# Kernel optimization log

Measured on AMD Instinct MI355X. Metric: run time of the kernel, lower is better.

The kernel has to match this reference:

```python
import jax, jax.numpy as jnp
import numpy as np

QMAX = 127.0

def quantize_int8(x):
    # symmetric per-row (per-token) int8 quantization
    scale = jnp.max(jnp.abs(x), axis=-1, keepdims=True) / QMAX  # [N,1]
    scale = jnp.maximum(scale, 1e-8)
    q = jnp.clip(jnp.round(x / scale), -QMAX, QMAX).astype(jnp.int8)
    return q, scale


def setup_inputs() -> dict:
    key = jax.random.key(0)
    k1, k2 = jax.random.split(key)
    in_features, out_features = 4096, 4096
    x = jax.random.normal(k1, (4, 2048, in_features), dtype=jnp.float32)
    # weight buffer: randint(1, 128) int8, shape (out, in)
    weight = jax.random.randint(k2, (out_features, in_features), 1, 128, dtype=jnp.int32).astype(jnp.int8)
    weight_scale = jnp.ones((1,), dtype=jnp.float32)
    return {"x": x, "weight": weight, "weight_scale": weight_scale}


def reference(x, weight, weight_scale):
    x_shape = x.shape
    xf = x.reshape(-1, x_shape[-1])  # [N, in]
    q, scale_x = quantize_int8(xf)
    acc = jnp.matmul(q, weight.T, preferred_element_type=jnp.int32)  # [N, out]
    y = acc.astype(jnp.float32) * scale_x * weight_scale[0]
    return y.reshape(*x_shape[:-1], -1)
```

## Files before the change

kernel.cpp:

```cpp
#include <hip/hip_runtime.h>
#include <cstdint>

typedef int v4i __attribute__((ext_vector_type(4)));

#define K_DIM 4096
#define BM 128
#define BN 128
#define BK 64

__global__ __launch_bounds__(256) void pack_weight(
    const int* __restrict__ w32, int8_t* __restrict__ w8, int total16)
{
    const int i = blockIdx.x * 256 + threadIdx.x;
    if (i >= total16) return;
    const v4i* src = reinterpret_cast<const v4i*>(w32) + i * 4;
    v4i out;
#pragma unroll
    for (int j = 0; j < 4; ++j) {
        const v4i v = src[j];
        out[j] = (v.x & 0xff) | ((v.y & 0xff) << 8) |
                 ((v.z & 0xff) << 16) | ((unsigned)(v.w & 0xff) << 24);
    }
    reinterpret_cast<v4i*>(w8)[i] = out;
}

__global__ __launch_bounds__(256) void quant_rows(
    const float* __restrict__ x, int8_t* __restrict__ q,
    float* __restrict__ scales)
{
    const int row = blockIdx.x;
    const int t   = threadIdx.x;
    const float4* xr4 = reinterpret_cast<const float4*>(x + (size_t)row * K_DIM);

    float4 v[4];
    float m = 0.0f;
#pragma unroll
    for (int i = 0; i < 4; ++i) {
        v[i] = xr4[i * 256 + t];
        m = fmaxf(m, fmaxf(fmaxf(fabsf(v[i].x), fabsf(v[i].y)),
                           fmaxf(fabsf(v[i].z), fabsf(v[i].w))));
    }
#pragma unroll
    for (int off = 32; off >= 1; off >>= 1)
        m = fmaxf(m, __shfl_xor(m, off, 64));

    __shared__ float wmax[4];
    if ((t & 63) == 0) wmax[t >> 6] = m;
    __syncthreads();
    const float am = fmaxf(fmaxf(wmax[0], wmax[1]), fmaxf(wmax[2], wmax[3]));
    const float s  = fmaxf(am / 127.0f, 1e-8f);
    if (t == 0) scales[row] = s;

    int* qi = reinterpret_cast<int*>(q + (size_t)row * K_DIM);
#pragma unroll
    for (int i = 0; i < 4; ++i) {
        const float e[4] = {v[i].x, v[i].y, v[i].z, v[i].w};
        unsigned packed = 0;
#pragma unroll
        for (int j = 0; j < 4; ++j) {
            float r = rintf(e[j] / s);
            r = fminf(fmaxf(r, -127.0f), 127.0f);
            packed |= ((unsigned)((int)r & 0xff)) << (8 * j);
        }
        qi[i * 256 + t] = (int)packed;
    }
}

__global__ __launch_bounds__(256, 2) void gemm_i8(
    const int8_t* __restrict__ A,
    const int8_t* __restrict__ B,
    const float* __restrict__ sA,
    const float* __restrict__ wsc,
    float* __restrict__ C,
    int M, int N)
{
    __shared__ int8_t ldsA[BM * BK];
    __shared__ int8_t ldsB[BN * BK];

    const int t    = threadIdx.x;
    const int lane = t & 63;
    const int wid  = t >> 6;
    const int wr   = wid >> 1;
    const int wc   = wid & 1;

    const int brow = blockIdx.y * BM;
    const int bcol = blockIdx.x * BN;

    const float ws = wsc[0];

    v4i acc[4][4];
#pragma unroll
    for (int i = 0; i < 4; ++i)
#pragma unroll
        for (int j = 0; j < 4; ++j)
            acc[i][j] = (v4i){0, 0, 0, 0};

    for (int kt = 0; kt < K_DIM; kt += BK) {
        __syncthreads();
#pragma unroll
        for (int b = 0; b < 2; ++b) {
            const int idx = b * 256 + t;
            const int row = idx >> 2;
            const int seg = (idx & 3) * 16;
            const int8_t* ga = A + (size_t)(brow + row) * K_DIM + kt + seg;
            const int8_t* gb = B + (size_t)(bcol + row) * K_DIM + kt + seg;
            __builtin_amdgcn_global_load_lds(
                (const __attribute__((address_space(1))) void*)ga,
                (__attribute__((address_space(3))) void*)(ldsA + idx * 16),
                16, 0, 0);
            __builtin_amdgcn_global_load_lds(
                (const __attribute__((address_space(1))) void*)gb,
                (__attribute__((address_space(3))) void*)(ldsB + idx * 16),
                16, 0, 0);
        }
        __syncthreads();

        v4i a[4], bf[4];
#pragma unroll
        for (int rb = 0; rb < 4; ++rb) {
            const int r = wr * 64 + rb * 16 + (lane & 15);
            a[rb] = *reinterpret_cast<const v4i*>(&ldsA[r * BK + (lane >> 4) * 16]);
        }
#pragma unroll
        for (int cb = 0; cb < 4; ++cb) {
            const int c = wc * 64 + cb * 16 + (lane & 15);
            bf[cb] = *reinterpret_cast<const v4i*>(&ldsB[c * BK + (lane >> 4) * 16]);
        }
#pragma unroll
        for (int rb = 0; rb < 4; ++rb)
#pragma unroll
            for (int cb = 0; cb < 4; ++cb)
                acc[rb][cb] = __builtin_amdgcn_mfma_i32_16x16x64_i8(
                    a[rb], bf[cb], acc[rb][cb], 0, 0, 0);
    }

#pragma unroll
    for (int rb = 0; rb < 4; ++rb) {
        const int rbase = brow + wr * 64 + rb * 16 + (lane >> 4) * 4;
        float sc[4];
#pragma unroll
        for (int j = 0; j < 4; ++j) sc[j] = sA[rbase + j] * ws;
#pragma unroll
        for (int cb = 0; cb < 4; ++cb) {
            const int col = bcol + wc * 64 + cb * 16 + (lane & 15);
#pragma unroll
            for (int j = 0; j < 4; ++j)
                C[(size_t)(rbase + j) * N + col] = (float)acc[rb][cb][j] * sc[j];
        }
    }
}

extern "C" void kernel_launch(void* const* d_in, const int* in_sizes, int n_in,
                              void* d_out, int out_size, void* d_ws, size_t ws_size,
                              hipStream_t stream) {
    const float* x      = (const float*)d_in[0];
    const int*   w32    = (const int*)d_in[1];
    const float* wscale = (const float*)d_in[2];
    float*       out    = (float*)d_out;

    const int M = in_sizes[0] / K_DIM;
    const int N = in_sizes[1] / K_DIM;

    int8_t* q      = (int8_t*)d_ws;
    float*  scales = (float*)((char*)d_ws + (size_t)M * K_DIM);
    int8_t* w8     = (int8_t*)((char*)d_ws + (size_t)M * K_DIM + (size_t)M * sizeof(float));

    const int total16 = (N * K_DIM) / 16;
    pack_weight<<<(total16 + 255) / 256, 256, 0, stream>>>(w32, w8, total16);

    quant_rows<<<M, 256, 0, stream>>>(x, q, scales);

    dim3 grid(N / BN, M / BM);
    gemm_i8<<<grid, 256, 0, stream>>>(q, w8, scales, wscale, out, M, N);
}
```

Before: 233.0 us.

## Triple-buffer int8 GEMM with larger swizzled tiles and fuse prep kernels

Merges the weight-pack and row-quantize kernels into one launch. Rewrites the GEMM to use 128x256 tiles with each wave owning a 64-column strip, a three-stage LDS ring fed by global_load_lds with partial vmcnt waits, XOR-swizzled LDS addressing, a 1D grid remapped across XCDs, and s_setprio around the MFMA block. The aims are to overlap global loads with compute, cut LDS bank conflicts and spread work for better L2 reuse. In exchange the larger LDS footprint and 32 accumulators per thread may lower occupancy.

```diff
diff --git a/kernel.cpp b/kernel.cpp
--- a/kernel.cpp
+++ b/kernel.cpp
@@ -4,65 +4,67 @@
 typedef int v4i __attribute__((ext_vector_type(4)));
 
 #define K_DIM 4096
-#define BM 128
-#define BN 128
-#define BK 64
-
-__global__ __launch_bounds__(256) void pack_weight(
-    const int* __restrict__ w32, int8_t* __restrict__ w8, int total16)
+#define QBM 128
+#define QBN 256
+#define QBK 64
+#define NT (K_DIM / QBK)
+#define ATILE (QBM * QBK)
+#define BTILE (QBN * QBK)
+#define QBUFS (ATILE + BTILE)
+#define QNBUF 3
+
+__global__ __launch_bounds__(256) void prep(
+    const float* __restrict__ x, int8_t* __restrict__ q,
+    float* __restrict__ scales,
+    const int* __restrict__ w32, int8_t* __restrict__ w8,
+    int qrows, int total16)
 {
-    const int i = blockIdx.x * 256 + threadIdx.x;
-    if (i >= total16) return;
-    const v4i* src = reinterpret_cast<const v4i*>(w32) + i * 4;
-    v4i out;
-#pragma unroll
-    for (int j = 0; j < 4; ++j) {
-        const v4i v = src[j];
-        out[j] = (v.x & 0xff) | ((v.y & 0xff) << 8) |
-                 ((v.z & 0xff) << 16) | ((unsigned)(v.w & 0xff) << 24);
-    }
-    reinterpret_cast<v4i*>(w8)[i] = out;
-}
-
-__global__ __launch_bounds__(256) void quant_rows(
-    const float* __restrict__ x, int8_t* __restrict__ q,
-    float* __restrict__ scales)
-{
-    const int row = blockIdx.x;
-    const int t   = threadIdx.x;
-    const float4* xr4 = reinterpret_cast<const float4*>(x + (size_t)row * K_DIM);
-
-    float4 v[4];
-    float m = 0.0f;
-#pragma unroll
-    for (int i = 0; i < 4; ++i) {
-        v[i] = xr4[i * 256 + t];
-        m = fmaxf(m, fmaxf(fmaxf(fabsf(v[i].x), fabsf(v[i].y)),
-                           fmaxf(fabsf(v[i].z), fabsf(v[i].w))));
-    }
-#pragma unroll
-    for (int off = 32; off >= 1; off >>= 1)
-        m = fmaxf(m, __shfl_xor(m, off, 64));
-
-    __shared__ float wmax[4];
-    if ((t & 63) == 0) wmax[t >> 6] = m;
-    __syncthreads();
-    const float am = fmaxf(fmaxf(wmax[0], wmax[1]), fmaxf(wmax[2], wmax[3]));
-    const float s  = fmaxf(am / 127.0f, 1e-8f);
-    if (t == 0) scales[row] = s;
-
-    int* qi = reinterpret_cast<int*>(q + (size_t)row * K_DIM);
-#pragma unroll
-    for (int i = 0; i < 4; ++i) {
-        const float e[4] = {v[i].x, v[i].y, v[i].z, v[i].w};
-        unsigned packed = 0;
+    const int b = blockIdx.x;
+    const int t = threadIdx.x;
+    if (b < qrows) {
+        const float4* xr4 = reinterpret_cast<const float4*>(x + (size_t)b * K_DIM);
+        float4 v[4];
+        float m = 0.0f;
+#pragma unroll
+        for (int i = 0; i < 4; ++i) {
+            v[i] = xr4[i * 256 + t];
+            m = fmaxf(m, fmaxf(fmaxf(fabsf(v[i].x), fabsf(v[i].y)),
+                               fmaxf(fabsf(v[i].z), fabsf(v[i].w))));
+        }
+#pragma unroll
+        for (int off = 32; off >= 1; off >>= 1)
+            m = fmaxf(m, __shfl_xor(m, off, 64));
+        __shared__ float wmax[4];
+        if ((t & 63) == 0) wmax[t >> 6] = m;
+        __syncthreads();
+        const float am = fmaxf(fmaxf(wmax[0], wmax[1]), fmaxf(wmax[2], wmax[3]));
+        const float s  = fmaxf(am / 127.0f, 1e-8f);
+        if (t == 0) scales[b] = s;
+        int* qi = reinterpret_cast<int*>(q + (size_t)b * K_DIM);
+#pragma unroll
+        for (int i = 0; i < 4; ++i) {
+            const float e[4] = {v[i].x, v[i].y, v[i].z, v[i].w};
+            unsigned packed = 0;
+#pragma unroll
+            for (int j = 0; j < 4; ++j) {
+                float r = rintf(e[j] / s);
+                r = fminf(fmaxf(r, -127.0f), 127.0f);
+                packed |= ((unsigned)((int)r & 0xff)) << (8 * j);
+            }
+            qi[i * 256 + t] = (int)packed;
+        }
+    } else {
+        const int i = (b - qrows) * 256 + t;
+        if (i >= total16) return;
+        const v4i* src = reinterpret_cast<const v4i*>(w32) + i * 4;
+        v4i out;
 #pragma unroll
         for (int j = 0; j < 4; ++j) {
-            float r = rintf(e[j] / s);
-            r = fminf(fmaxf(r, -127.0f), 127.0f);
-            packed |= ((unsigned)((int)r & 0xff)) << (8 * j);
-        }
-        qi[i * 256 + t] = (int)packed;
+            const v4i vv = src[j];
+            out[j] = (vv.x & 0xff) | ((vv.y & 0xff) << 8) |
+                     ((vv.z & 0xff) << 16) | ((unsigned)(vv.w & 0xff) << 24);
+        }
+        reinterpret_cast<v4i*>(w8)[i] = out;
     }
 }
 
@@ -74,80 +76,117 @@
     float* __restrict__ C,
     int M, int N)
 {
-    __shared__ int8_t ldsA[BM * BK];
-    __shared__ int8_t ldsB[BN * BK];
+    __shared__ int8_t lds[QNBUF * QBUFS];
 
     const int t    = threadIdx.x;
     const int lane = t & 63;
-    const int wid  = t >> 6;
-    const int wr   = wid >> 1;
-    const int wc   = wid & 1;
-
-    const int brow = blockIdx.y * BM;
-    const int bcol = blockIdx.x * BN;
-
-    const float ws = wsc[0];
-
-    v4i acc[4][4];
-#pragma unroll
-    for (int i = 0; i < 4; ++i)
-#pragma unroll
-        for (int j = 0; j < 4; ++j)
-            acc[i][j] = (v4i){0, 0, 0, 0};
-
-    for (int kt = 0; kt < K_DIM; kt += BK) {
-        __syncthreads();
-#pragma unroll
-        for (int b = 0; b < 2; ++b) {
-            const int idx = b * 256 + t;
-            const int row = idx >> 2;
-            const int seg = (idx & 3) * 16;
-            const int8_t* ga = A + (size_t)(brow + row) * K_DIM + kt + seg;
-            const int8_t* gb = B + (size_t)(bcol + row) * K_DIM + kt + seg;
-            __builtin_amdgcn_global_load_lds(
-                (const __attribute__((address_space(1))) void*)ga,
-                (__attribute__((address_space(3))) void*)(ldsA + idx * 16),
-                16, 0, 0);
-            __builtin_amdgcn_global_load_lds(
-                (const __attribute__((address_space(1))) void*)gb,
-                (__attribute__((address_space(3))) void*)(ldsB + idx * 16),
-                16, 0, 0);
-        }
-        __syncthreads();
-
-        v4i a[4], bf[4];
-#pragma unroll
-        for (int rb = 0; rb < 4; ++rb) {
-            const int r = wr * 64 + rb * 16 + (lane & 15);
-            a[rb] = *reinterpret_cast<const v4i*>(&ldsA[r * BK + (lane >> 4) * 16]);
-        }
-#pragma unroll
-        for (int cb = 0; cb < 4; ++cb) {
-            const int c = wc * 64 + cb * 16 + (lane & 15);
-            bf[cb] = *reinterpret_cast<const v4i*>(&ldsB[c * BK + (lane >> 4) * 16]);
-        }
-#pragma unroll
-        for (int rb = 0; rb < 4; ++rb)
-#pragma unroll
-            for (int cb = 0; cb < 4; ++cb)
-                acc[rb][cb] = __builtin_amdgcn_mfma_i32_16x16x64_i8(
-                    a[rb], bf[cb], acc[rb][cb], 0, 0, 0);
-    }
-
-#pragma unroll
-    for (int rb = 0; rb < 4; ++rb) {
-        const int rbase = brow + wr * 64 + rb * 16 + (lane >> 4) * 4;
+    const int wc   = t >> 6;
+
+    const int nwg = gridDim.x;
+    int bid = blockIdx.x;
+    if ((nwg & 7) == 0) bid = (bid & 7) * (nwg >> 3) + (bid >> 3);
+    const int ntn  = N / QBN;
+    const int brow = (bid / ntn) * QBM;
+    const int bcol = (bid % ntn) * QBN;
+
+    const int8_t* gsA[2]; int ldA[2];
+    const int8_t* gsB[4]; int ldB[4];
+#pragma unroll
+    for (int c = 0; c < 2; ++c) {
+        const int idx = c * 256 + t;
+        const int row = idx >> 2;
+        const int col = (((idx & 3) ^ ((row >> 1) & 3)) << 4);
+        gsA[c] = A + (size_t)(brow + row) * K_DIM + col;
+        ldA[c] = idx * 16;
+    }
+#pragma unroll
+    for (int c = 0; c < 4; ++c) {
+        const int idx = c * 256 + t;
+        const int row = idx >> 2;
+        const int col = (((idx & 3) ^ ((row >> 1) & 3)) << 4);
+        gsB[c] = B + (size_t)(bcol + row) * K_DIM + col;
+        ldB[c] = ATILE + idx * 16;
+    }
+
+#define GLDS(gp, off) \
+    __builtin_amdgcn_global_load_lds( \
+        (const __attribute__((address_space(1))) void*)(gp), \
+        (__attribute__((address_space(3))) void*)(lds + (off)), 16, 0, 0)
+#define STAGE(bf, tt) do { \
+    GLDS(gsA[0] + (size_t)(tt) * QBK, (bf) * QBUFS + ldA[0]); \
+    GLDS(gsA[1] + (size_t)(tt) * QBK, (bf) * QBUFS + ldA[1]); \
+    GLDS(gsB[0] + (size_t)(tt) * QBK, (bf) * QBUFS + ldB[0]); \
+    GLDS(gsB[1] + (size_t)(tt) * QBK, (bf) * QBUFS + ldB[1]); \
+    GLDS(gsB[2] + (size_t)(tt) * QBK, (bf) * QBUFS + ldB[2]); \
+    GLDS(gsB[3] + (size_t)(tt) * QBK, (bf) * QBUFS + ldB[3]); } while (0)
+
+    const int l15 = lane & 15;
+    const unsigned swz = ((unsigned)((lane >> 4) ^ ((l15 >> 1) & 3))) << 4;
+    const unsigned vA = (unsigned)(l15 * QBK) + swz;
+    const unsigned vB = (unsigned)(ATILE + (wc * 64 + l15) * QBK) + swz;
+
+    v4i acc[8][4];
+#pragma unroll
+    for (int m = 0; m < 8; ++m)
+#pragma unroll
+        for (int n = 0; n < 4; ++n)
+            acc[m][n] = (v4i){0, 0, 0, 0};
+
+    STAGE(0, 0);
+    STAGE(1, 1);
+    asm volatile("s_waitcnt vmcnt(6)" ::: "memory");
+    __builtin_amdgcn_s_barrier();
+
+    int cur = 0;
+    for (int tt = 0; tt < NT; ++tt) {
+        const int8_t* bufc = lds + cur * QBUFS;
+        int nx2 = cur + 2; if (nx2 >= QNBUF) nx2 -= QNBUF;
+        const bool more    = tt + 2 < NT;
+        const bool notlast = tt + 1 < NT;
+
+        if (more) STAGE(nx2, tt + 2);
+
+        v4i af[8], bf[4];
+#pragma unroll
+        for (int m = 0; m < 8; ++m)
+            af[m] = *(const v4i*)(bufc + vA + m * 1024);
+#pragma unroll
+        for (int n = 0; n < 4; ++n)
+            bf[n] = *(const v4i*)(bufc + vB + n * 1024);
+
+        __builtin_amdgcn_s_setprio(1);
+#pragma unroll
+        for (int m = 0; m < 8; ++m)
+#pragma unroll
+            for (int n = 0; n < 4; ++n)
+                acc[m][n] = __builtin_amdgcn_mfma_i32_16x16x64_i8(
+                    af[m], bf[n], acc[m][n], 0, 0, 0);
+        __builtin_amdgcn_s_setprio(0);
+
+        if (more)         asm volatile("s_waitcnt vmcnt(6)" ::: "memory");
+        else if (notlast) asm volatile("s_waitcnt vmcnt(0)" ::: "memory");
+        if (notlast) __builtin_amdgcn_s_barrier();
+
+        cur = cur + 1; if (cur >= QNBUF) cur -= QNBUF;
+    }
+
+    const float wsv = wsc[0];
+#pragma unroll
+    for (int m = 0; m < 8; ++m) {
+        const int rbase = brow + m * 16 + (lane >> 4) * 4;
         float sc[4];
 #pragma unroll
-        for (int j = 0; j < 4; ++j) sc[j] = sA[rbase + j] * ws;
-#pragma unroll
-        for (int cb = 0; cb < 4; ++cb) {
-            const int col = bcol + wc * 64 + cb * 16 + (lane & 15);
+        for (int j = 0; j < 4; ++j) sc[j] = sA[rbase + j] * wsv;
+#pragma unroll
+        for (int n = 0; n < 4; ++n) {
+            const int col = bcol + wc * 64 + n * 16 + l15;
 #pragma unroll
             for (int j = 0; j < 4; ++j)
-                C[(size_t)(rbase + j) * N + col] = (float)acc[rb][cb][j] * sc[j];
-        }
-    }
+                C[(size_t)(rbase + j) * N + col] = (float)acc[m][n][j] * sc[j];
+        }
+    }
+#undef GLDS
+#undef STAGE
 }
 
 extern "C" void kernel_launch(void* const* d_in, const int* in_sizes, int n_in,
@@ -166,10 +205,9 @@
     int8_t* w8     = (int8_t*)((char*)d_ws + (size_t)M * K_DIM + (size_t)M * sizeof(float));
 
     const int total16 = (N * K_DIM) / 16;
-    pack_weight<<<(total16 + 255) / 256, 256, 0, stream>>>(w32, w8, total16);
-
-    quant_rows<<<M, 256, 0, stream>>>(x, q, scales);
-
-    dim3 grid(N / BN, M / BM);
-    gemm_i8<<<grid, 256, 0, stream>>>(q, w8, scales, wscale, out, M, N);
+    const int pblocks = (total16 + 255) / 256;
+    prep<<<M + pblocks, 256, 0, stream>>>(x, q, scales, w32, w8, M, total16);
+
+    const int nblk = (M / QBM) * (N / QBN);
+    gemm_i8<<<nblk, 256, 0, stream>>>(q, w8, scales, wscale, out, M, N);
 }
```

Result: faster. 205.2 us (-11.9%).
